# Kernel optimization log

Hardware: AMD Instinct MI355X
Metric: run time of the kernel (lower is better)

The kernel has to match this reference:

```python
import math
import jax, jax.numpy as jnp
import numpy as np

SCALES = (128.0, 256.0, 512.0)
ASPECT_RATIOS = (0.5, 1.0, 2.0)
NMS_THR = 0.7
PRENMS_K = 6000   # rpn_test_prenms_topk (module built with training=False)
POST_K = 300      # rpn_test_topk
MIN_SIZE = 16.0
DW_CLIP = math.log(1000.0 / 16.0)


def conv2d(x, w, b, pad):
    y = jax.lax.conv_general_dilated(
        x, w, window_strides=(1, 1), padding=[(pad, pad), (pad, pad)],
        dimension_numbers=("NCHW", "OIHW", "NCHW"))
    return y + b[None, :, None, None]


def generate_anchors(im_h, im_w, grid_h, grid_w, dtype):
    stride_h = float(im_h // grid_h)
    stride_w = float(im_w // grid_w)
    ar = jnp.asarray(ASPECT_RATIOS, dtype)
    sc = jnp.asarray(SCALES, dtype)
    h_ratios = jnp.sqrt(ar)
    w_ratios = 1.0 / h_ratios
    hs = (h_ratios[:, None] * sc[None, :]).reshape(-1)   # [A]
    ws = (w_ratios[:, None] * sc[None, :]).reshape(-1)
    base = jnp.round(jnp.stack([-ws, -hs, ws, hs], axis=1) / 2.0)  # [A,4]
    xs = jnp.arange(grid_w, dtype=dtype) * stride_w
    ys = jnp.arange(grid_h, dtype=dtype) * stride_h
    sy, sx = jnp.meshgrid(ys, xs, indexing="ij")
    sx = sx.reshape(-1); sy = sy.reshape(-1)
    shift = jnp.stack([sx, sy, sx, sy], axis=1)           # [HW,4]
    return (shift[:, None, :] + base[None, :, :]).reshape(-1, 4)  # [HW*A,4]


def decode_boxes(pred, anchors):
    # pred, anchors: [N,4] -> decoded [N,4]
    w = anchors[:, 2] - anchors[:, 0]
    h = anchors[:, 3] - anchors[:, 1]
    cx = anchors[:, 0] + 0.5 * w
    cy = anchors[:, 1] + 0.5 * h
    dx, dy = pred[:, 0], pred[:, 1]
    dw = jnp.minimum(pred[:, 2], DW_CLIP)
    dh = jnp.minimum(pred[:, 3], DW_CLIP)
    px = dx * w + cx
    py = dy * h + cy
    pw = jnp.exp(dw) * w
    ph = jnp.exp(dh) * h
    return jnp.stack([px - 0.5 * pw, py - 0.5 * ph, px + 0.5 * pw, py + 0.5 * ph], axis=1)


def nms_keep(boxes, valid, thr):
    # boxes assumed sorted by descending score; sequential greedy NMS.
    N = boxes.shape[0]
    area = (boxes[:, 2] - boxes[:, 0]) * (boxes[:, 3] - boxes[:, 1])
    idx = jnp.arange(N)

    def body(i, keep):
        b = jax.lax.dynamic_slice(boxes, (i, 0), (1, 4))[0]
        x1 = jnp.maximum(b[0], boxes[:, 0])
        y1 = jnp.maximum(b[1], boxes[:, 1])
        x2 = jnp.minimum(b[2], boxes[:, 2])
        y2 = jnp.minimum(b[3], boxes[:, 3])
        inter = jnp.clip(x2 - x1, 0.0) * jnp.clip(y2 - y1, 0.0)
        iou = inter / (area[i] + area - inter)
        suppress = (iou > thr) & (idx > i) & keep[i]
        return keep & ~suppress

    return jax.lax.fori_loop(0, N, body, valid)


def rpn_forward(image, feat, rpn_conv_w, rpn_conv_b, cls_w, cls_b, bbox_w, bbox_b):
    rpn_feat = jax.nn.relu(conv2d(feat, rpn_conv_w, rpn_conv_b, pad=1))
    cls_scores = conv2d(rpn_feat, cls_w, cls_b, pad=0)       # [B,A,H,W]
    box_pred = conv2d(rpn_feat, bbox_w, bbox_b, pad=0)       # [B,4A,H,W]
    B, A, H, W = cls_scores.shape
    im_h, im_w = image.shape[-2], image.shape[-1]
    anchors = generate_anchors(im_h, im_w, H, W, feat.dtype)  # [HWA,4]

    cls_flat = jnp.transpose(cls_scores, (0, 2, 3, 1)).reshape(-1)              # [B*H*W*A]
    pred = jnp.transpose(box_pred.reshape(B, A, 4, H, W), (0, 3, 4, 1, 2)).reshape(-1, 4)
    proposals = decode_boxes(pred, anchors)                   # [N,4]

    scores = jax.nn.sigmoid(cls_flat)
    top_scores, top_idx = jax.lax.top_k(scores, PRENMS_K)
    props = proposals[top_idx]                                # [K,4]
    # clamp to image boundary
    props = jnp.stack([
        jnp.clip(props[:, 0], 0.0, float(im_w)),
        jnp.clip(props[:, 1], 0.0, float(im_h)),
        jnp.clip(props[:, 2], 0.0, float(im_w)),
        jnp.clip(props[:, 3], 0.0, float(im_h))], axis=1)
    w = props[:, 2] - props[:, 0]
    h = props[:, 3] - props[:, 1]
    valid = (w >= MIN_SIZE) & (h >= MIN_SIZE)
    keep = nms_keep(props, valid, NMS_THR)                    # already score-sorted
    masked = jnp.where(keep, top_scores, -jnp.inf)
    final_scores, sel = jax.lax.top_k(masked, POST_K)
    final_boxes = props[sel]
    ok = jnp.isfinite(final_scores)
    final_boxes = jnp.where(ok[:, None], final_boxes, 0.0)
    final_scores = jnp.where(ok, final_scores, 0.0)
    return jnp.concatenate([final_boxes, final_scores[:, None]], axis=1)  # [POST_K,5]


def setup_inputs() -> dict:
    key = jax.random.key(0)
    ks = jax.random.split(key, 6)
    C, H, W, A = 256, 128, 128, 9
    IMH = IMW = 1024
    std = 0.01
    return {
        "image": jax.random.normal(ks[0], (1, 3, IMH, IMW), jnp.float32),
        "feat": jax.random.normal(ks[1], (1, C, H, W), jnp.float32),
        "rpn_conv_w": jax.random.normal(ks[2], (C, C, 3, 3), jnp.float32) * std,
        "rpn_conv_b": jnp.zeros((C,), jnp.float32),
        "cls_w": jax.random.normal(ks[3], (A, C, 1, 1), jnp.float32) * std,
        "cls_b": jnp.zeros((A,), jnp.float32),
        "bbox_w": jax.random.normal(ks[4], (4 * A, C, 1, 1), jnp.float32) * std,
        "bbox_b": jnp.zeros((4 * A,), jnp.float32),
    }


def reference(image, feat, rpn_conv_w, rpn_conv_b, cls_w, cls_b, bbox_w, bbox_b):
    return rpn_forward(image, feat, rpn_conv_w, rpn_conv_b, cls_w, cls_b, bbox_w, bbox_b)
```

## Files before the change

kernel.cpp:

```cpp
#include <hip/hip_runtime.h>

#define HW 128
#define NPIX 16384
#define CIN 256
#define NSC 147456
#define PRENMS 6000
#define POSTK 300
#define DW_CLIP_F 4.135166556742356f
#define MW 96
typedef unsigned long long ull;

__global__ void prep_kernel(const float* __restrict__ w, float* __restrict__ wt,
                            unsigned* __restrict__ zp, int nz) {
    int i = blockIdx.x * 256 + threadIdx.x;
    if (i < nz) zp[i] = 0u;
    if (i < 2304 * 256) {
        int k = i >> 8, co = i & 255;
        wt[i] = w[co * 2304 + k];
    }
}

__global__ __launch_bounds__(256) void conv3x3_half_kernel(
    const float* __restrict__ feat, const float* __restrict__ wt,
    float* __restrict__ part)
{
    __shared__ float in_s[8 * 324];
    const int tx = threadIdx.x;
    const int ty = threadIdx.y;
    const int x0 = blockIdx.x * 16;
    const int y0 = blockIdx.y * 16;
    const int h  = blockIdx.z >> 4;
    const int co0 = (blockIdx.z & 15) << 4;
    const int tid = ty * 16 + tx;

    const int yy1 = tid / 18, xx1 = tid - yy1 * 18;
    const int t2 = tid + 256;
    const int yy2 = t2 / 18, xx2 = t2 - yy2 * 18;
    const int gy1 = y0 + yy1 - 1, gx1 = x0 + xx1 - 1;
    const int gy2 = y0 + yy2 - 1, gx2 = x0 + xx2 - 1;
    const bool p1 = ((unsigned)gy1 < 128u) && ((unsigned)gx1 < 128u);
    const bool p2 = (tid < 68) && ((unsigned)gy2 < 128u) && ((unsigned)gx2 < 128u);
    const int a1 = p1 ? (gy1 * 128 + gx1) : 0;
    const int a2 = p2 ? (gy2 * 128 + gx2) : 0;

    float acc[16];
#pragma unroll
    for (int i = 0; i < 16; ++i) acc[i] = 0.f;

    const float* fh = feat + h * 128 * NPIX;
    const float* wh = wt + h * 128 * 9 * 256;

    for (int s = 0; s < 16; ++s) {
        __syncthreads();
        const float* fbase = fh + s * 8 * NPIX;
#pragma unroll
        for (int ci = 0; ci < 8; ++ci) {
            float t = fbase[ci * NPIX + a1];
            in_s[ci * 324 + tid] = p1 ? t : 0.f;
        }
        if (tid < 68) {
#pragma unroll
            for (int ci = 0; ci < 8; ++ci) {
                float t = fbase[ci * NPIX + a2];
                in_s[ci * 324 + 256 + tid] = p2 ? t : 0.f;
            }
        }
        __syncthreads();
        const float* ws0 = wh + s * 8 * 9 * 256 + co0;
#pragma unroll 4
        for (int ci = 0; ci < 8; ++ci) {
            const float* wrow = ws0 + ci * 9 * 256;
#pragma unroll
            for (int t = 0; t < 9; ++t) {
                const int ky = t / 3, kx = t - ky * 3;
                float v = in_s[ci * 324 + (ty + ky) * 18 + (tx + kx)];
                const float* wp = wrow + t * 256;
#pragma unroll
                for (int co = 0; co < 16; ++co)
                    acc[co] = fmaf(v, wp[co], acc[co]);
            }
        }
    }
    float* po = part + h * (CIN * NPIX) + co0 * NPIX + (y0 + ty) * 128 + (x0 + tx);
#pragma unroll
    for (int co = 0; co < 16; ++co)
        po[co * NPIX] = acc[co];
}

__global__ __launch_bounds__(64) void heads_kernel(
    const float* __restrict__ part, const float* __restrict__ conv_b,
    const float* __restrict__ cls_w, const float* __restrict__ cls_b,
    const float* __restrict__ bbox_w, const float* __restrict__ bbox_b,
    float* __restrict__ scores, float* __restrict__ bb)
{
    __shared__ float wl[256][48];
    const int tid = threadIdx.x;
    for (int e = tid; e < 256 * 45; e += 64) {
        int s = e >> 8, ci = e & 255;
        wl[ci][s] = (s < 9) ? cls_w[s * CIN + ci] : bbox_w[(s - 9) * CIN + ci];
    }
    __syncthreads();

    const int p = blockIdx.x * 64 + tid;
    const float* p0 = part + p;
    const float* p1s = part + CIN * NPIX + p;
    float acc[45];
#pragma unroll
    for (int i = 0; i < 45; ++i) acc[i] = 0.f;

    float va[4], vb[4];
#pragma unroll
    for (int k = 0; k < 4; ++k) { va[k] = p0[k * NPIX]; vb[k] = p1s[k * NPIX]; }

#pragma unroll 4
    for (int ci = 0; ci < CIN; ++ci) {
        float v = fmaxf(va[ci & 3] + vb[ci & 3] + conv_b[ci], 0.f);
        if (ci + 4 < CIN) {
            va[ci & 3] = p0[(ci + 4) * NPIX];
            vb[ci & 3] = p1s[(ci + 4) * NPIX];
        }
        const float4* wr = (const float4*)&wl[ci][0];
#pragma unroll
        for (int q = 0; q < 11; ++q) {
            float4 w4 = wr[q];
            acc[q * 4 + 0] = fmaf(v, w4.x, acc[q * 4 + 0]);
            acc[q * 4 + 1] = fmaf(v, w4.y, acc[q * 4 + 1]);
            acc[q * 4 + 2] = fmaf(v, w4.z, acc[q * 4 + 2]);
            acc[q * 4 + 3] = fmaf(v, w4.w, acc[q * 4 + 3]);
        }
        acc[44] = fmaf(v, wl[ci][44], acc[44]);
    }
#pragma unroll
    for (int a = 0; a < 9; ++a) {
        float s = acc[a] + cls_b[a];
        scores[p * 9 + a] = 1.0f / (1.0f + expf(-s));
    }
#pragma unroll
    for (int c = 0; c < 36; ++c) {
        bb[c * NPIX + p] = acc[9 + c] + bbox_b[c];
    }
}

__global__ __launch_bounds__(1024) void hist1_kernel(const float* __restrict__ scores,
                                                     unsigned* __restrict__ hist1) {
    __shared__ unsigned h[16384];
    const int tid = threadIdx.x;
    for (int i = tid; i < 16384; i += 1024) h[i] = 0u;
    __syncthreads();
    for (int i = blockIdx.x * 1024 + tid; i < NSC; i += gridDim.x * 1024) {
        unsigned bits = __float_as_uint(scores[i]);
        atomicAdd(&h[bits >> 16], 1u);
    }
    __syncthreads();
    for (int i = tid; i < 16384; i += 1024) {
        unsigned c = h[i];
        if (c) atomicAdd(&hist1[i], c);
    }
}

__global__ __launch_bounds__(1024) void scan1_kernel(const unsigned* __restrict__ hist,
                                                     unsigned* __restrict__ meta) {
    __shared__ unsigned ssum[1024];
    const int t = threadIdx.x;
    unsigned local[16];
    unsigned s = 0;
#pragma unroll
    for (int i = 0; i < 16; ++i) { local[i] = hist[t * 16 + i]; s += local[i]; }
    ssum[t] = s;
    __syncthreads();
    for (int off = 1; off < 1024; off <<= 1) {
        unsigned v = ssum[t] + ((t + off < 1024) ? ssum[t + off] : 0u);
        __syncthreads();
        ssum[t] = v;
        __syncthreads();
    }
    unsigned run = ssum[t] - s;
#pragma unroll
    for (int i = 15; i >= 0; --i) {
        unsigned nb = run + local[i];
        if (nb >= (unsigned)PRENMS && run < (unsigned)PRENMS) {
            meta[1] = (unsigned)(t * 16 + i);
            meta[2] = run;
        }
        run = nb;
    }
}

__global__ void hist2_kernel(const float* __restrict__ scores, const unsigned* __restrict__ meta,
                             unsigned* __restrict__ hist2) {
    int i = blockIdx.x * 256 + threadIdx.x;
    if (i < NSC) {
        unsigned bits = __float_as_uint(scores[i]);
        if ((bits >> 16) == meta[1]) atomicAdd(&hist2[bits & 0xFFFFu], 1u);
    }
}

__global__ __launch_bounds__(1024) void scan2_kernel(const unsigned* __restrict__ hist2,
                                                     unsigned* __restrict__ meta) {
    __shared__ unsigned ssum[1024];
    const int t = threadIdx.x;
    const unsigned need = (unsigned)PRENMS - meta[2];
    unsigned s = 0;
    for (int i = 0; i < 64; ++i) s += hist2[t * 64 + i];
    ssum[t] = s;
    __syncthreads();
    for (int off = 1; off < 1024; off <<= 1) {
        unsigned v = ssum[t] + ((t + off < 1024) ? ssum[t + off] : 0u);
        __syncthreads();
        ssum[t] = v;
        __syncthreads();
    }
    unsigned run = ssum[t] - s;
    for (int i = 63; i >= 0; --i) {
        unsigned h = hist2[t * 64 + i];
        unsigned nb = run + h;
        if (nb >= need && run < need) {
            meta[3] = (meta[1] << 16) | (unsigned)(t * 64 + i);
        }
        run = nb;
    }
}

__global__ void compact_kernel(const float* __restrict__ scores, unsigned* __restrict__ meta,
                               ull* __restrict__ cand) {
    int i = blockIdx.x * 256 + threadIdx.x;
    unsigned bits = (i < NSC) ? __float_as_uint(scores[i]) : 0u;
    bool pred = (i < NSC) && (bits >= meta[3]);
    ull bal = __ballot(pred);
    int lane = threadIdx.x & 63;
    unsigned cnt = (unsigned)__popcll(bal);
    unsigned base = 0;
    if (lane == 0 && cnt) base = atomicAdd(&meta[0], cnt);
    base = __shfl(base, 0);
    if (pred) {
        unsigned off = (unsigned)__popcll(bal & ((1ull << lane) - 1ull));
        unsigned pos = base + off;
        if (pos < 8192u)
            cand[pos] = ((ull)bits << 32) | (unsigned)(~i);
    }
}

__global__ __launch_bounds__(1024) void sortA_kernel(const ull* __restrict__ cand,
                                                     const unsigned* __restrict__ meta,
                                                     ull* __restrict__ sorted) {
    __shared__ ull keys[2048];
    const int tid = threadIdx.x;
    const int base = blockIdx.x * 2048;
    const int n = min((int)meta[0], 8192);
    for (int i = tid; i < 2048; i += 1024) {
        int g = base + i;
        keys[i] = (g < n) ? cand[g] : (ull)(8191 - g);
    }
    __syncthreads();
    for (int k = 2; k <= 2048; k <<= 1) {
        for (int j = k >> 1; j >= 1; j >>= 1) {
            int s = tid;
            int i = ((s & ~(j - 1)) << 1) | (s & (j - 1));
            int p = i | j;
            ull a = keys[i], c = keys[p];
            bool desc = ((i & k) == 0);
            bool sw = desc ? (a < c) : (a > c);
            if (sw) { keys[i] = c; keys[p] = a; }
            __syncthreads();
        }
    }
    for (int i = tid; i < 2048; i += 1024) sorted[base + i] = keys[i];
}

__global__ __launch_bounds__(256) void merge_kernel(const ull* __restrict__ sorted,
                                                    ull* __restrict__ fin) {
    const int g = blockIdx.x * 256 + threadIdx.x;
    ull x = sorted[g];
    const int c = g >> 11;
    int rank = g & 2047;
#pragma unroll
    for (int cc = 0; cc < 4; ++cc) {
        if (cc == c) continue;
        const ull* arr = sorted + cc * 2048;
        int lo = 0, hi = 2048;
        while (lo < hi) { int mid = (lo + hi) >> 1; if (arr[mid] > x) lo = mid + 1; else hi = mid; }
        rank += lo;
    }
    fin[rank] = x;
}

__global__ __launch_bounds__(64) void decode_kernel(
    const ull* __restrict__ fin, const float* __restrict__ bb,
    float* __restrict__ selbox, float* __restrict__ selsc,
    ull* __restrict__ validbits)
{
    const int r = blockIdx.x * 64 + threadIdx.x;
    int valid = 0;
    if (r < PRENMS) {
        ull key = fin[r];
        unsigned sbits = (unsigned)(key >> 32);
        unsigned idx = ~(unsigned)(key & 0xFFFFFFFFull);
        float score = __uint_as_float(sbits);
        int p = (int)(idx / 9u);
        int a = (int)(idx - (unsigned)p * 9u);
        int y = p >> 7, x = p & 127;
        float d0 = bb[(a * 4 + 0) * NPIX + p];
        float d1 = bb[(a * 4 + 1) * NPIX + p];
        float d2 = bb[(a * 4 + 2) * NPIX + p];
        float d3 = bb[(a * 4 + 3) * NPIX + p];
        int ar_i = a / 3, sc_i = a - ar_i * 3;
        float arv = (ar_i == 0) ? 0.5f : ((ar_i == 1) ? 1.0f : 2.0f);
        float scv = (sc_i == 0) ? 128.f : ((sc_i == 1) ? 256.f : 512.f);
        float hr = sqrtf(arv);
        float wr = 1.0f / hr;
        float hs = hr * scv;
        float wsv = wr * scv;
        float bx1 = rintf(-wsv * 0.5f), by1 = rintf(-hs * 0.5f);
        float bx2 = rintf(wsv * 0.5f),  by2 = rintf(hs * 0.5f);
        float ax1 = x * 8.f + bx1, ay1 = y * 8.f + by1;
        float ax2 = x * 8.f + bx2, ay2 = y * 8.f + by2;
        float wa = ax2 - ax1, ha = ay2 - ay1;
        float cx = ax1 + 0.5f * wa, cy = ay1 + 0.5f * ha;
        float dw = fminf(d2, DW_CLIP_F), dh = fminf(d3, DW_CLIP_F);
        float px = d0 * wa + cx, py = d1 * ha + cy;
        float pw = expf(dw) * wa, ph = expf(dh) * ha;
        float x1 = px - 0.5f * pw, y1 = py - 0.5f * ph;
        float x2 = px + 0.5f * pw, y2 = py + 0.5f * ph;
        x1 = fminf(fmaxf(x1, 0.f), 1024.f);
        y1 = fminf(fmaxf(y1, 0.f), 1024.f);
        x2 = fminf(fmaxf(x2, 0.f), 1024.f);
        y2 = fminf(fmaxf(y2, 0.f), 1024.f);
        float bw = x2 - x1, bh = y2 - y1;
        valid = (bw >= 16.f) && (bh >= 16.f);
        selbox[r * 4 + 0] = x1; selbox[r * 4 + 1] = y1;
        selbox[r * 4 + 2] = x2; selbox[r * 4 + 3] = y2;
        selsc[r] = score;
    }
    ull bal = __ballot(valid);
    if (threadIdx.x == 0) validbits[blockIdx.x] = bal;
}

__global__ __launch_bounds__(256) void maskbuild_kernel(
    const float* __restrict__ selbox, ull* __restrict__ mask)
{
    __shared__ float jb0[64], jb1[64], jb2[64], jb3[64];
    const int jw = blockIdx.y;
    const int tid = threadIdx.x;
    const int i = blockIdx.x * 256 + tid;
    if (jw * 64 + 63 < blockIdx.x * 256) {
        if (i < PRENMS) mask[(size_t)i * MW + jw] = 0ull;
        return;
    }
    if (tid < 64) {
        int j = jw * 64 + tid;
        float x1 = 0.f, y1 = 0.f, x2 = 0.f, y2 = 0.f;
        if (j < PRENMS) {
            x1 = selbox[j * 4 + 0]; y1 = selbox[j * 4 + 1];
            x2 = selbox[j * 4 + 2]; y2 = selbox[j * 4 + 3];
        }
        jb0[tid] = x1; jb1[tid] = y1; jb2[tid] = x2; jb3[tid] = y2;
    }
    __syncthreads();
    if (i >= PRENMS) return;
    const float ix1 = selbox[i * 4 + 0], iy1 = selbox[i * 4 + 1];
    const float ix2 = selbox[i * 4 + 2], iy2 = selbox[i * 4 + 3];
    const float iarea = (ix2 - ix1) * (iy2 - iy1);
    ull word = 0ull;
    for (int b = 0; b < 64; ++b) {
        int j = jw * 64 + b;
        float xx1 = fmaxf(ix1, jb0[b]);
        float yy1 = fmaxf(iy1, jb1[b]);
        float xx2 = fminf(ix2, jb2[b]);
        float yy2 = fminf(iy2, jb3[b]);
        float iw = fmaxf(xx2 - xx1, 0.f);
        float ih = fmaxf(yy2 - yy1, 0.f);
        float inter = iw * ih;
        float jarea = (jb2[b] - jb0[b]) * (jb3[b] - jb1[b]);
        float iou = inter / (iarea + jarea - inter);
        if (j > i && iou > 0.7f) word |= (1ull << b);
    }
    mask[(size_t)i * MW + jw] = word;
}

__global__ __launch_bounds__(64) void nms_scan_kernel(
    const ull* __restrict__ validbits,
    const ull* __restrict__ mask,
    const float* __restrict__ selbox, const float* __restrict__ selsc,
    float* __restrict__ out)
{
    __shared__ int kept[POSTK];
    const int l = threadIdx.x;
    ull supp0 = ~validbits[l];
    ull supp1 = (l < 30) ? ~validbits[64 + l] : ~0ull;
    int nk = 0;
    ull ownrow_next = mask[(size_t)l * MW + 0];
    for (int wi = 0; wi < 94 && nk < POSTK; ++wi) {
        ull ownrow = ownrow_next;
        if (wi < 93) ownrow_next = mask[(size_t)((wi + 1) * 64 + l) * MW + (wi + 1)];
        ull wsup = (wi < 64) ? __shfl(supp0, wi) : __shfl(supp1, wi - 64);
        ull active = ~wsup;
        if (!active) continue;
        ull keptbits = 0ull;
        while (active && nk < POSTK) {
            int b = __builtin_ctzll(active);
            keptbits |= (1ull << b);
            if (l == 0) kept[nk] = wi * 64 + b;
            nk++;
            ull rowb = __shfl(ownrow, b);
            ull gt = (b == 63) ? 0ull : (~0ull << (b + 1));
            active &= gt & ~rowb;
        }
        while (keptbits) {
            int b0 = __builtin_ctzll(keptbits); keptbits &= keptbits - 1;
            int b1 = -1, b2 = -1, b3 = -1;
            if (keptbits) { b1 = __builtin_ctzll(keptbits); keptbits &= keptbits - 1; }
            if (keptbits) { b2 = __builtin_ctzll(keptbits); keptbits &= keptbits - 1; }
            if (keptbits) { b3 = __builtin_ctzll(keptbits); keptbits &= keptbits - 1; }
            const ull* r0 = mask + (size_t)(wi * 64 + b0) * MW;
            ull t0a = r0[l], t0b = (l < 30) ? r0[64 + l] : 0ull;
            ull t1a = 0, t1b = 0, t2a = 0, t2b = 0, t3a = 0, t3b = 0;
            if (b1 >= 0) { const ull* r1 = mask + (size_t)(wi * 64 + b1) * MW; t1a = r1[l]; t1b = (l < 30) ? r1[64 + l] : 0ull; }
            if (b2 >= 0) { const ull* r2 = mask + (size_t)(wi * 64 + b2) * MW; t2a = r2[l]; t2b = (l < 30) ? r2[64 + l] : 0ull; }
            if (b3 >= 0) { const ull* r3 = mask + (size_t)(wi * 64 + b3) * MW; t3a = r3[l]; t3b = (l < 30) ? r3[64 + l] : 0ull; }
            supp0 |= t0a | t1a | t2a | t3a;
            supp1 |= t0b | t1b | t2b | t3b;
        }
    }
    __syncthreads();
    for (int r = l; r < POSTK; r += 64) {
        if (r < nk) {
            int i = kept[r];
            out[r * 5 + 0] = selbox[i * 4 + 0];
            out[r * 5 + 1] = selbox[i * 4 + 1];
            out[r * 5 + 2] = selbox[i * 4 + 2];
            out[r * 5 + 3] = selbox[i * 4 + 3];
            out[r * 5 + 4] = selsc[i];
        } else {
            out[r * 5 + 0] = 0.f; out[r * 5 + 1] = 0.f;
            out[r * 5 + 2] = 0.f; out[r * 5 + 3] = 0.f;
            out[r * 5 + 4] = 0.f;
        }
    }
}

extern "C" void kernel_launch(void* const* d_in, const int* in_sizes, int n_in,
                              void* d_out, int out_size, void* d_ws, size_t ws_size,
                              hipStream_t stream) {
    const float* feat    = (const float*)d_in[1];
    const float* conv_w  = (const float*)d_in[2];
    const float* conv_b  = (const float*)d_in[3];
    const float* cls_w   = (const float*)d_in[4];
    const float* cls_b   = (const float*)d_in[5];
    const float* bbox_w  = (const float*)d_in[6];
    const float* bbox_b  = (const float*)d_in[7];
    float* out = (float*)d_out;

    char* ws = (char*)d_ws;
    float*    part      = (float*)(ws + 0);
    float*    wt        = (float*)(ws + 33554432);
    float*    bb        = (float*)(ws + 35913728);
    float*    scores    = (float*)(ws + 38273024);
    unsigned* hist1     = (unsigned*)(ws + 38862848);
    unsigned* hist2     = (unsigned*)(ws + 38928384);
    unsigned* meta      = (unsigned*)(ws + 39190528);
    ull*      cand      = (ull*)(ws + 39190784);
    ull*      sorted    = (ull*)(ws + 39256320);
    ull*      fin       = (ull*)(ws + 39321856);
    float*    selbox    = (float*)(ws + 39387392);
    float*    selsc    = (float*)(ws + 39483648);
    ull*      validbits = (ull*)(ws + 39507712);
    ull*      mask      = (ull*)(ws + 39508480);

    const int nz = 16384 + 65536 + 64;
    prep_kernel<<<(2304 * 256 + 255) / 256, 256, 0, stream>>>(conv_w, wt, hist1, nz);
    conv3x3_half_kernel<<<dim3(8, 8, 32), dim3(16, 16), 0, stream>>>(feat, wt, part);
    heads_kernel<<<256, 64, 0, stream>>>(part, conv_b, cls_w, cls_b, bbox_w, bbox_b, scores, bb);
    hist1_kernel<<<64, 1024, 0, stream>>>(scores, hist1);
    scan1_kernel<<<1, 1024, 0, stream>>>(hist1, meta);
    hist2_kernel<<<(NSC + 255) / 256, 256, 0, stream>>>(scores, meta, hist2);
    scan2_kernel<<<1, 1024, 0, stream>>>(hist2, meta);
    compact_kernel<<<(NSC + 255) / 256, 256, 0, stream>>>(scores, meta, cand);
    sortA_kernel<<<4, 1024, 0, stream>>>(cand, meta, sorted);
    merge_kernel<<<32, 256, 0, stream>>>(sorted, fin);
    decode_kernel<<<94, 64, 0, stream>>>(fin, bb, selbox, selsc, validbits);
    maskbuild_kernel<<<dim3(24, 94), 256, 0, stream>>>(selbox, mask);
    nms_scan_kernel<<<1, 64, 0, stream>>>(validbits, mask, selbox, selsc, out);
}
```

Before: 629.8 us.

## Retile conv to single-wave blocks, split heads reduction, fuse merge with decode

The 3x3 conv now uses 64-thread blocks covering a 16x4 pixel tile with a padded 19-wide LDS row. It drops all __syncthreads and relies on single-wavefront lockstep execution. The heads kernel splits the 256 input channels across four waves and reduces the partial sums through LDS. It reads a pre-transposed 45-wide weight table built in prep_kernel instead of staging weights per block. The merge and decode kernels are fused: each sorted key computes its rank and decodes its box directly, setting valid bits with atomicOr into a zero-initialised buffer. The intent is more parallelism and fewer launches and barriers, at the cost of less LDS reuse per conv block and reliance on implicit wave synchronisation.

```diff
diff --git a/kernel.cpp b/kernel.cpp
--- a/kernel.cpp
+++ b/kernel.cpp
@@ -11,133 +11,143 @@
 typedef unsigned long long ull;
 
 __global__ void prep_kernel(const float* __restrict__ w, float* __restrict__ wt,
+                            const float* __restrict__ cls_w, const float* __restrict__ bbox_w,
+                            float* __restrict__ wh45,
                             unsigned* __restrict__ zp, int nz) {
     int i = blockIdx.x * 256 + threadIdx.x;
     if (i < nz) zp[i] = 0u;
+    if (i < 11520) {
+        int ci = i / 45, s = i - ci * 45;
+        wh45[i] = (s < 9) ? cls_w[s * CIN + ci] : bbox_w[(s - 9) * CIN + ci];
+    }
     if (i < 2304 * 256) {
         int k = i >> 8, co = i & 255;
         wt[i] = w[co * 2304 + k];
     }
 }
 
-__global__ __launch_bounds__(256) void conv3x3_half_kernel(
+__global__ __launch_bounds__(64, 8) void conv3x3_kernel(
     const float* __restrict__ feat, const float* __restrict__ wt,
     float* __restrict__ part)
 {
-    __shared__ float in_s[8 * 324];
-    const int tx = threadIdx.x;
-    const int ty = threadIdx.y;
-    const int x0 = blockIdx.x * 16;
-    const int y0 = blockIdx.y * 16;
-    const int h  = blockIdx.z >> 4;
-    const int co0 = (blockIdx.z & 15) << 4;
-    const int tid = ty * 16 + tx;
-
-    const int yy1 = tid / 18, xx1 = tid - yy1 * 18;
-    const int t2 = tid + 256;
-    const int yy2 = t2 / 18, xx2 = t2 - yy2 * 18;
-    const int gy1 = y0 + yy1 - 1, gx1 = x0 + xx1 - 1;
-    const int gy2 = y0 + yy2 - 1, gx2 = x0 + xx2 - 1;
-    const bool p1 = ((unsigned)gy1 < 128u) && ((unsigned)gx1 < 128u);
-    const bool p2 = (tid < 68) && ((unsigned)gy2 < 128u) && ((unsigned)gx2 < 128u);
-    const int a1 = p1 ? (gy1 * 128 + gx1) : 0;
-    const int a2 = p2 ? (gy2 * 128 + gx2) : 0;
+    __shared__ float in_s[8 * 114];
+    const int l = threadIdx.x;
+    const int sp = blockIdx.x;
+    const int x0 = (sp & 7) * 16;
+    const int y0 = (sp >> 3) * 4;
+    const int co0 = blockIdx.y * 16;
+    const int h = blockIdx.z;
+    const int tx = l & 15, ty = l >> 4;
+
+    const int r1 = l / 18, c1 = l - r1 * 18;
+    const int e2 = l + 64;
+    const int r2 = e2 / 18, c2 = e2 - r2 * 18;
+    const int gy1 = y0 + r1 - 1, gx1 = x0 + c1 - 1;
+    const int gy2 = y0 + r2 - 1, gx2 = x0 + c2 - 1;
+    const bool q1 = ((unsigned)gy1 < 128u) && ((unsigned)gx1 < 128u);
+    const bool q2 = (l < 44) && ((unsigned)gy2 < 128u) && ((unsigned)gx2 < 128u);
+    const int a1 = q1 ? (gy1 * 128 + gx1) : 0;
+    const int a2 = q2 ? (gy2 * 128 + gx2) : 0;
+    const int d1 = r1 * 19 + c1;
+    const int d2 = r2 * 19 + c2;
 
     float acc[16];
 #pragma unroll
     for (int i = 0; i < 16; ++i) acc[i] = 0.f;
 
     const float* fh = feat + h * 128 * NPIX;
-    const float* wh = wt + h * 128 * 9 * 256;
+    const float* whp = wt + h * 128 * 9 * 256 + co0;
 
     for (int s = 0; s < 16; ++s) {
-        __syncthreads();
-        const float* fbase = fh + s * 8 * NPIX;
+        const float* fb = fh + s * 8 * NPIX;
 #pragma unroll
         for (int ci = 0; ci < 8; ++ci) {
-            float t = fbase[ci * NPIX + a1];
-            in_s[ci * 324 + tid] = p1 ? t : 0.f;
-        }
-        if (tid < 68) {
-#pragma unroll
-            for (int ci = 0; ci < 8; ++ci) {
-                float t = fbase[ci * NPIX + a2];
-                in_s[ci * 324 + 256 + tid] = p2 ? t : 0.f;
+            float f1 = fb[ci * NPIX + a1];
+            in_s[ci * 114 + d1] = q1 ? f1 : 0.f;
+            if (l < 44) {
+                float f2 = fb[ci * NPIX + a2];
+                in_s[ci * 114 + d2] = q2 ? f2 : 0.f;
             }
         }
-        __syncthreads();
-        const float* ws0 = wh + s * 8 * 9 * 256 + co0;
-#pragma unroll 4
+        const float* ws0 = whp + s * 8 * 9 * 256;
+#pragma unroll
         for (int ci = 0; ci < 8; ++ci) {
-            const float* wrow = ws0 + ci * 9 * 256;
 #pragma unroll
             for (int t = 0; t < 9; ++t) {
                 const int ky = t / 3, kx = t - ky * 3;
-                float v = in_s[ci * 324 + (ty + ky) * 18 + (tx + kx)];
-                const float* wp = wrow + t * 256;
+                float v = in_s[ci * 114 + (ty + ky) * 19 + (tx + kx)];
+                const float* wp = ws0 + (ci * 9 + t) * 256;
 #pragma unroll
                 for (int co = 0; co < 16; ++co)
                     acc[co] = fmaf(v, wp[co], acc[co]);
             }
         }
     }
-    float* po = part + h * (CIN * NPIX) + co0 * NPIX + (y0 + ty) * 128 + (x0 + tx);
+    float* po = part + h * (CIN * NPIX) + co0 * NPIX + (y0 + ty) * 128 + x0 + tx;
 #pragma unroll
     for (int co = 0; co < 16; ++co)
         po[co * NPIX] = acc[co];
 }
 
-__global__ __launch_bounds__(64) void heads_kernel(
+__global__ __launch_bounds__(256) void heads_kernel(
     const float* __restrict__ part, const float* __restrict__ conv_b,
-    const float* __restrict__ cls_w, const float* __restrict__ cls_b,
-    const float* __restrict__ bbox_w, const float* __restrict__ bbox_b,
+    const float* __restrict__ wh45,
+    const float* __restrict__ cls_b, const float* __restrict__ bbox_b,
     float* __restrict__ scores, float* __restrict__ bb)
 {
-    __shared__ float wl[256][48];
-    const int tid = threadIdx.x;
-    for (int e = tid; e < 256 * 45; e += 64) {
-        int s = e >> 8, ci = e & 255;
-        wl[ci][s] = (s < 9) ? cls_w[s * CIN + ci] : bbox_w[(s - 9) * CIN + ci];
-    }
-    __syncthreads();
-
-    const int p = blockIdx.x * 64 + tid;
+    __shared__ float partial[3][64][46];
+    const int t = threadIdx.x;
+    const int lane = t & 63, q = t >> 6;
+    const int p = blockIdx.x * 64 + lane;
     const float* p0 = part + p;
-    const float* p1s = part + CIN * NPIX + p;
+    const float* p1 = part + CIN * NPIX + p;
+    const int cb = q * 64;
+
     float acc[45];
 #pragma unroll
     for (int i = 0; i < 45; ++i) acc[i] = 0.f;
 
     float va[4], vb[4];
 #pragma unroll
-    for (int k = 0; k < 4; ++k) { va[k] = p0[k * NPIX]; vb[k] = p1s[k * NPIX]; }
-
+    for (int k = 0; k < 4; ++k) {
+        va[k] = p0[(cb + k) * NPIX];
+        vb[k] = p1[(cb + k) * NPIX];
+    }
 #pragma unroll 4
-    for (int ci = 0; ci < CIN; ++ci) {
-        float v = fmaxf(va[ci & 3] + vb[ci & 3] + conv_b[ci], 0.f);
-        if (ci + 4 < CIN) {
-            va[ci & 3] = p0[(ci + 4) * NPIX];
-            vb[ci & 3] = p1s[(ci + 4) * NPIX];
-        }
-        const float4* wr = (const float4*)&wl[ci][0];
-#pragma unroll
-        for (int q = 0; q < 11; ++q) {
-            float4 w4 = wr[q];
-            acc[q * 4 + 0] = fmaf(v, w4.x, acc[q * 4 + 0]);
-            acc[q * 4 + 1] = fmaf(v, w4.y, acc[q * 4 + 1]);
-            acc[q * 4 + 2] = fmaf(v, w4.z, acc[q * 4 + 2]);
-            acc[q * 4 + 3] = fmaf(v, w4.w, acc[q * 4 + 3]);
-        }
-        acc[44] = fmaf(v, wl[ci][44], acc[44]);
-    }
-#pragma unroll
-    for (int a = 0; a < 9; ++a) {
-        float s = acc[a] + cls_b[a];
-        scores[p * 9 + a] = 1.0f / (1.0f + expf(-s));
-    }
-#pragma unroll
-    for (int c = 0; c < 36; ++c) {
-        bb[c * NPIX + p] = acc[9 + c] + bbox_b[c];
+    for (int i = 0; i < 64; ++i) {
+        const int ci = cb + i;
+        float v = fmaxf(va[i & 3] + vb[i & 3] + conv_b[ci], 0.f);
+        if (i + 4 < 64) {
+            va[i & 3] = p0[(ci + 4) * NPIX];
+            vb[i & 3] = p1[(ci + 4) * NPIX];
+        }
+        const float* wr = wh45 + ci * 45;
+#pragma unroll
+        for (int s = 0; s < 45; ++s)
+            acc[s] = fmaf(v, wr[s], acc[s]);
+    }
+    if (q) {
+#pragma unroll
+        for (int s = 0; s < 45; ++s) partial[q - 1][lane][s] = acc[s];
+    }
+    __syncthreads();
+    if (q == 0) {
+#pragma unroll
+        for (int s = 0; s < 45; ++s) {
+            float r = acc[s] + partial[0][lane][s];
+            r += partial[1][lane][s];
+            r += partial[2][lane][s];
+            acc[s] = r;
+        }
+#pragma unroll
+        for (int a = 0; a < 9; ++a) {
+            float s = acc[a] + cls_b[a];
+            scores[p * 9 + a] = 1.0f / (1.0f + expf(-s));
+        }
+#pragma unroll
+        for (int c = 0; c < 36; ++c) {
+            bb[c * NPIX + p] = acc[9 + c] + bbox_b[c];
+        }
     }
 }
 
@@ -267,10 +277,13 @@
     for (int i = tid; i < 2048; i += 1024) sorted[base + i] = keys[i];
 }
 
-__global__ __launch_bounds__(256) void merge_kernel(const ull* __restrict__ sorted,
-                                                    ull* __restrict__ fin) {
+__global__ __launch_bounds__(256) void merge_decode_kernel(
+    const ull* __restrict__ sorted, const float* __restrict__ bb,
+    float* __restrict__ selbox, float* __restrict__ selsc,
+    ull* __restrict__ validbits)
+{
     const int g = blockIdx.x * 256 + threadIdx.x;
-    ull x = sorted[g];
+    ull key = sorted[g];
     const int c = g >> 11;
     int rank = g & 2047;
 #pragma unroll
@@ -278,61 +291,48 @@
         if (cc == c) continue;
         const ull* arr = sorted + cc * 2048;
         int lo = 0, hi = 2048;
-        while (lo < hi) { int mid = (lo + hi) >> 1; if (arr[mid] > x) lo = mid + 1; else hi = mid; }
+        while (lo < hi) { int mid = (lo + hi) >> 1; if (arr[mid] > key) lo = mid + 1; else hi = mid; }
         rank += lo;
     }
-    fin[rank] = x;
-}
-
-__global__ __launch_bounds__(64) void decode_kernel(
-    const ull* __restrict__ fin, const float* __restrict__ bb,
-    float* __restrict__ selbox, float* __restrict__ selsc,
-    ull* __restrict__ validbits)
-{
-    const int r = blockIdx.x * 64 + threadIdx.x;
-    int valid = 0;
-    if (r < PRENMS) {
-        ull key = fin[r];
-        unsigned sbits = (unsigned)(key >> 32);
-        unsigned idx = ~(unsigned)(key & 0xFFFFFFFFull);
-        float score = __uint_as_float(sbits);
-        int p = (int)(idx / 9u);
-        int a = (int)(idx - (unsigned)p * 9u);
-        int y = p >> 7, x = p & 127;
-        float d0 = bb[(a * 4 + 0) * NPIX + p];
-        float d1 = bb[(a * 4 + 1) * NPIX + p];
-        float d2 = bb[(a * 4 + 2) * NPIX + p];
-        float d3 = bb[(a * 4 + 3) * NPIX + p];
-        int ar_i = a / 3, sc_i = a - ar_i * 3;
-        float arv = (ar_i == 0) ? 0.5f : ((ar_i == 1) ? 1.0f : 2.0f);
-        float scv = (sc_i == 0) ? 128.f : ((sc_i == 1) ? 256.f : 512.f);
-        float hr = sqrtf(arv);
-        float wr = 1.0f / hr;
-        float hs = hr * scv;
-        float wsv = wr * scv;
-        float bx1 = rintf(-wsv * 0.5f), by1 = rintf(-hs * 0.5f);
-        float bx2 = rintf(wsv * 0.5f),  by2 = rintf(hs * 0.5f);
-        float ax1 = x * 8.f + bx1, ay1 = y * 8.f + by1;
-        float ax2 = x * 8.f + bx2, ay2 = y * 8.f + by2;
-        float wa = ax2 - ax1, ha = ay2 - ay1;
-        float cx = ax1 + 0.5f * wa, cy = ay1 + 0.5f * ha;
-        float dw = fminf(d2, DW_CLIP_F), dh = fminf(d3, DW_CLIP_F);
-        float px = d0 * wa + cx, py = d1 * ha + cy;
-        float pw = expf(dw) * wa, ph = expf(dh) * ha;
-        float x1 = px - 0.5f * pw, y1 = py - 0.5f * ph;
-        float x2 = px + 0.5f * pw, y2 = py + 0.5f * ph;
-        x1 = fminf(fmaxf(x1, 0.f), 1024.f);
-        y1 = fminf(fmaxf(y1, 0.f), 1024.f);
-        x2 = fminf(fmaxf(x2, 0.f), 1024.f);
-        y2 = fminf(fmaxf(y2, 0.f), 1024.f);
-        float bw = x2 - x1, bh = y2 - y1;
-        valid = (bw >= 16.f) && (bh >= 16.f);
-        selbox[r * 4 + 0] = x1; selbox[r * 4 + 1] = y1;
-        selbox[r * 4 + 2] = x2; selbox[r * 4 + 3] = y2;
-        selsc[r] = score;
-    }
-    ull bal = __ballot(valid);
-    if (threadIdx.x == 0) validbits[blockIdx.x] = bal;
+    if (rank >= PRENMS) return;
+    unsigned sbits = (unsigned)(key >> 32);
+    unsigned idx = ~(unsigned)(key & 0xFFFFFFFFull);
+    float score = __uint_as_float(sbits);
+    int p = (int)(idx / 9u);
+    int a = (int)(idx - (unsigned)p * 9u);
+    int y = p >> 7, x = p & 127;
+    float d0 = bb[(a * 4 + 0) * NPIX + p];
+    float d1 = bb[(a * 4 + 1) * NPIX + p];
+    float d2 = bb[(a * 4 + 2) * NPIX + p];
+    float d3 = bb[(a * 4 + 3) * NPIX + p];
+    int ar_i = a / 3, sc_i = a - ar_i * 3;
+    float arv = (ar_i == 0) ? 0.5f : ((ar_i == 1) ? 1.0f : 2.0f);
+    float scv = (sc_i == 0) ? 128.f : ((sc_i == 1) ? 256.f : 512.f);
+    float hr = sqrtf(arv);
+    float wr = 1.0f / hr;
+    float hs = hr * scv;
+    float wsv = wr * scv;
+    float bx1 = rintf(-wsv * 0.5f), by1 = rintf(-hs * 0.5f);
+    float bx2 = rintf(wsv * 0.5f),  by2 = rintf(hs * 0.5f);
+    float ax1 = x * 8.f + bx1, ay1 = y * 8.f + by1;
+    float ax2 = x * 8.f + bx2, ay2 = y * 8.f + by2;
+    float wa = ax2 - ax1, ha = ay2 - ay1;
+    float cx = ax1 + 0.5f * wa, cy = ay1 + 0.5f * ha;
+    float dw = fminf(d2, DW_CLIP_F), dh = fminf(d3, DW_CLIP_F);
+    float px = d0 * wa + cx, py = d1 * ha + cy;
+    float pw = expf(dw) * wa, ph = expf(dh) * ha;
+    float x1 = px - 0.5f * pw, y1 = py - 0.5f * ph;
+    float x2 = px + 0.5f * pw, y2 = py + 0.5f * ph;
+    x1 = fminf(fmaxf(x1, 0.f), 1024.f);
+    y1 = fminf(fmaxf(y1, 0.f), 1024.f);
+    x2 = fminf(fmaxf(x2, 0.f), 1024.f);
+    y2 = fminf(fmaxf(y2, 0.f), 1024.f);
+    float bw = x2 - x1, bh = y2 - y1;
+    selbox[rank * 4 + 0] = x1; selbox[rank * 4 + 1] = y1;
+    selbox[rank * 4 + 2] = x2; selbox[rank * 4 + 3] = y2;
+    selsc[rank] = score;
+    if ((bw >= 16.f) && (bh >= 16.f))
+        atomicOr(&validbits[rank >> 6], 1ull << (rank & 63));
 }
 
 __global__ __launch_bounds__(256) void maskbuild_kernel(
@@ -453,31 +453,30 @@
     char* ws = (char*)d_ws;
     float*    part      = (float*)(ws + 0);
     float*    wt        = (float*)(ws + 33554432);
-    float*    bb        = (float*)(ws + 35913728);
-    float*    scores    = (float*)(ws + 38273024);
-    unsigned* hist1     = (unsigned*)(ws + 38862848);
-    unsigned* hist2     = (unsigned*)(ws + 38928384);
-    unsigned* meta      = (unsigned*)(ws + 39190528);
-    ull*      cand      = (ull*)(ws + 39190784);
-    ull*      sorted    = (ull*)(ws + 39256320);
-    ull*      fin       = (ull*)(ws + 39321856);
-    float*    selbox    = (float*)(ws + 39387392);
-    float*    selsc    = (float*)(ws + 39483648);
-    ull*      validbits = (ull*)(ws + 39507712);
-    ull*      mask      = (ull*)(ws + 39508480);
-
-    const int nz = 16384 + 65536 + 64;
-    prep_kernel<<<(2304 * 256 + 255) / 256, 256, 0, stream>>>(conv_w, wt, hist1, nz);
-    conv3x3_half_kernel<<<dim3(8, 8, 32), dim3(16, 16), 0, stream>>>(feat, wt, part);
-    heads_kernel<<<256, 64, 0, stream>>>(part, conv_b, cls_w, cls_b, bbox_w, bbox_b, scores, bb);
+    float*    wh45      = (float*)(ws + 35913728);
+    float*    bb        = (float*)(ws + 35959808);
+    float*    scores    = (float*)(ws + 38319104);
+    unsigned* hist1     = (unsigned*)(ws + 38908928);
+    unsigned* hist2     = (unsigned*)(ws + 38974464);
+    unsigned* meta      = (unsigned*)(ws + 39236608);
+    ull*      validbits = (ull*)(ws + 39236864);
+    ull*      cand      = (ull*)(ws + 39237632);
+    ull*      sorted    = (ull*)(ws + 39303168);
+    float*    selbox    = (float*)(ws + 39368704);
+    float*    selsc     = (float*)(ws + 39464960);
+    ull*      mask      = (ull*)(ws + 39489024);
+
+    const int nz = 16384 + 65536 + 64 + 192;
+    prep_kernel<<<2304, 256, 0, stream>>>(conv_w, wt, cls_w, bbox_w, wh45, hist1, nz);
+    conv3x3_kernel<<<dim3(256, 16, 2), 64, 0, stream>>>(feat, wt, part);
+    heads_kernel<<<256, 256, 0, stream>>>(part, conv_b, wh45, cls_b, bbox_b, scores, bb);
     hist1_kernel<<<64, 1024, 0, stream>>>(scores, hist1);
     scan1_kernel<<<1, 1024, 0, stream>>>(hist1, meta);
     hist2_kernel<<<(NSC + 255) / 256, 256, 0, stream>>>(scores, meta, hist2);
     scan2_kernel<<<1, 1024, 0, stream>>>(hist2, meta);
     compact_kernel<<<(NSC + 255) / 256, 256, 0, stream>>>(scores, meta, cand);
     sortA_kernel<<<4, 1024, 0, stream>>>(cand, meta, sorted);
-    merge_kernel<<<32, 256, 0, stream>>>(sorted, fin);
-    decode_kernel<<<94, 64, 0, stream>>>(fin, bb, selbox, selsc, validbits);
+    merge_decode_kernel<<<32, 256, 0, stream>>>(sorted, bb, selbox, selsc, validbits);
     maskbuild_kernel<<<dim3(24, 94), 256, 0, stream>>>(selbox, mask);
     nms_scan_kernel<<<1, 64, 0, stream>>>(validbits, mask, selbox, selsc, out);
 }
```

Measured after the change: 597.3 us. 5.2% less time.
